# Optimization experiments

Measured on AMD Instinct MI355X. Metric: run time of the kernel, lower is better.

## Reference

```python
import jax, jax.numpy as jnp
import numpy as np

B, N, D, H, DH = 4, 4096, 1024, 8, 64
INNER = H * DH
EPS = 1e-5


def setup_inputs() -> dict:
    key = jax.random.key(0)
    ks = jax.random.split(key, 8)
    x = jax.random.normal(ks[0], (B, N, D), dtype=jnp.float32)
    W_qkv = jax.random.normal(ks[1], (3 * INNER, D), dtype=jnp.float32) * 0.02
    gamma_q = 1.0 + 0.1 * jax.random.normal(ks[2], (H, DH), dtype=jnp.float32)
    beta_q = 0.1 * jax.random.normal(ks[3], (H, DH), dtype=jnp.float32)
    gamma_k = 1.0 + 0.1 * jax.random.normal(ks[4], (H, DH), dtype=jnp.float32)
    beta_k = 0.1 * jax.random.normal(ks[5], (H, DH), dtype=jnp.float32)
    W_out = jax.random.normal(ks[6], (D, INNER), dtype=jnp.float32) * 0.02
    b_out = jnp.zeros((D,), dtype=jnp.float32)
    return {"x": x, "W_qkv": W_qkv, "gamma_q": gamma_q, "beta_q": beta_q,
            "gamma_k": gamma_k, "beta_k": beta_k, "W_out": W_out, "b_out": b_out}


def _per_head_layernorm(t, gamma, beta):
    # t: [B, H, N, DH]; gamma/beta: [H, DH] (one LayerNorm per head)
    m = jnp.mean(t, axis=-1, keepdims=True)
    var = jnp.mean(jnp.square(t - m), axis=-1, keepdims=True)
    tn = (t - m) * jax.lax.rsqrt(var + EPS)
    return tn * gamma[None, :, None, :] + beta[None, :, None, :]


def reference(x, W_qkv, gamma_q, beta_q, gamma_k, beta_k, W_out, b_out):
    b, n, d = x.shape
    h, dh = gamma_q.shape
    qkv = x @ W_qkv.T                                   # [B, N, 3*H*DH]
    q, k, v = jnp.split(qkv, 3, axis=-1)
    to_heads = lambda t: t.reshape(b, n, h, dh).transpose(0, 2, 1, 3)  # [B,H,N,DH]
    q, k, v = to_heads(q), to_heads(k), to_heads(v)
    q = _per_head_layernorm(q, gamma_q, beta_q)
    k = _per_head_layernorm(k, gamma_k, beta_k)
    # Softmax-free Galerkin attention: (Q K^T V) / (sqrt(dh) * n) reassociated
    # as Q (K^T V) -- mathematically identical, linear in n.
    scale = 1.0 / (jnp.sqrt(jnp.asarray(dh, x.dtype)) * n)
    kv = jnp.einsum('bhnd,bhne->bhde', k, v)            # [B,H,DH,DH]
    out = jnp.einsum('bhnd,bhde->bhne', q, kv) * scale  # [B,H,N,DH]
    out = out.transpose(0, 2, 1, 3).reshape(b, n, h * dh)
    return out @ W_out.T + b_out
```

## Files before the change

### kernel.cpp

```cpp
#include <hip/hip_runtime.h>
#include <stdint.h>

typedef unsigned short u16;
typedef unsigned int u32;
typedef __bf16 bf16x8 __attribute__((ext_vector_type(8)));
typedef float f32x4 __attribute__((ext_vector_type(4)));

__device__ __forceinline__ float bf2f(u16 u) {
  return __builtin_bit_cast(float, (u32)u << 16);
}
__device__ __forceinline__ u16 f2b(float f) {
  u32 u = __builtin_bit_cast(u32, f);
  u32 r = (u + 0x7fffu + ((u >> 16) & 1u)) >> 16;
  return (u16)r;
}
__device__ __forceinline__ void gload16(const u16* g, u16* l) {
  __builtin_amdgcn_global_load_lds(
      (const __attribute__((address_space(1))) u32*)(const void*)g,
      (__attribute__((address_space(3))) u32*)(void*)l, 16, 0, 0);
}
__device__ __forceinline__ void unpack16(uint4 a, uint4 b, float* o) {
  u32 w[8] = {a.x, a.y, a.z, a.w, b.x, b.y, b.z, b.w};
#pragma unroll
  for (int i = 0; i < 8; ++i) {
    o[2 * i]     = __builtin_bit_cast(float, w[i] << 16);
    o[2 * i + 1] = __builtin_bit_cast(float, w[i] & 0xffff0000u);
  }
}

__global__ __launch_bounds__(256) void cvt_bf16(const float* __restrict__ in,
                                                u16* __restrict__ out, int n4) {
  int i = blockIdx.x * 256 + threadIdx.x;
  if (i >= n4) return;
  float4 v = reinterpret_cast<const float4*>(in)[i];
  ushort4 o;
  o.x = f2b(v.x); o.y = f2b(v.y); o.z = f2b(v.z); o.w = f2b(v.w);
  reinterpret_cast<ushort4*>(out)[i] = o;
}

template <int MODE>
__global__ __launch_bounds__(256, 3) void gemm_bt(
    const u16* __restrict__ A, const u16* __restrict__ B, void* __restrict__ C,
    const float* __restrict__ gq, const float* __restrict__ bq,
    const float* __restrict__ gk, const float* __restrict__ bk,
    const float* __restrict__ bias, int M, int N, int K, int ntn) {
  __shared__ u16 As[2][128 * 32];
  __shared__ u16 Bs[2][128 * 32];

  const int nwg = gridDim.x;
  const int bid0 = blockIdx.x;
  const int bid = (bid0 & 7) * (nwg >> 3) + (bid0 >> 3);
  const int tm = bid / ntn, tn = bid % ntn;
  const int brow = tm << 7, bcol = tn << 7;
  const int tid = threadIdx.x;
  const int w = tid >> 6, lane = tid & 63;
  const int wrow = (w >> 1) << 6, wcol = (w & 1) << 6;
  const int lr = lane & 15, lg = lane >> 4;

  const int sslot = (lane & 3) ^ ((lane >> 3) & 3);
  const u16* Asrc = A + (size_t)(brow + (lane >> 2)) * K + sslot * 8;
  const u16* Bsrc = B + (size_t)(bcol + (lane >> 2)) * K + sslot * 8;

  auto stage = [&](int t, int buf) {
    const int k0 = t << 5;
#pragma unroll
    for (int i = 0; i < 2; ++i) {
      int g = w + 4 * i;
      gload16(Asrc + (size_t)(16 * g) * K + k0, &As[buf][(16 * g) * 32]);
      gload16(Bsrc + (size_t)(16 * g) * K + k0, &Bs[buf][(16 * g) * 32]);
    }
  };

  f32x4 acc[4][4];
#pragma unroll
  for (int m = 0; m < 4; ++m)
#pragma unroll
    for (int n = 0; n < 4; ++n) acc[m][n] = (f32x4){0.f, 0.f, 0.f, 0.f};

  const int NC = K >> 5;
  const int kslot = (lg ^ ((lr >> 1) & 3)) << 3;

  stage(0, 0);
  __syncthreads();

  for (int t = 0; t < NC; ++t) {
    const int cur = t & 1;
    if (t + 1 < NC) stage(t + 1, cur ^ 1);

    const u16* Asb = As[cur];
    const u16* Bsb = Bs[cur];
    bf16x8 af[4], bfr[4];
#pragma unroll
    for (int m = 0; m < 4; ++m)
      af[m] = *reinterpret_cast<const bf16x8*>(&Asb[(wrow + m * 16 + lr) * 32 + kslot]);
#pragma unroll
    for (int n = 0; n < 4; ++n)
      bfr[n] = *reinterpret_cast<const bf16x8*>(&Bsb[(wcol + n * 16 + lr) * 32 + kslot]);
    __builtin_amdgcn_s_setprio(1);
#pragma unroll
    for (int m = 0; m < 4; ++m)
#pragma unroll
      for (int n = 0; n < 4; ++n)
        acc[m][n] = __builtin_amdgcn_mfma_f32_16x16x32_bf16(af[m], bfr[n], acc[m][n], 0, 0, 0);
    __builtin_amdgcn_s_setprio(0);
    __syncthreads();
  }

  const int orow = brow + wrow + ((lane >> 4) << 2);
  const int ocol = bcol + wcol + lr;
  if (MODE == 0) {
    const int wcol0 = bcol + wcol;
    const int sect = wcol0 >> 6;
    const bool doln = sect < 16;
    const float* Gp = (sect < 8) ? (gq + wcol0) : (gk + (wcol0 - 512));
    const float* Pp = (sect < 8) ? (bq + wcol0) : (bk + (wcol0 - 512));
    float gv[4], pv[4];
    if (doln) {
#pragma unroll
      for (int n = 0; n < 4; ++n) { gv[n] = Gp[n * 16 + lr]; pv[n] = Pp[n * 16 + lr]; }
    }
    u16* Cp = (u16*)C;
#pragma unroll
    for (int m = 0; m < 4; ++m)
#pragma unroll
      for (int r = 0; r < 4; ++r) {
        size_t rowoff = (size_t)(orow + m * 16 + r) * N;
        if (doln) {
          float s = 0.f, s2 = 0.f;
#pragma unroll
          for (int n = 0; n < 4; ++n) {
            float x = acc[m][n][r];
            s += x; s2 += x * x;
          }
#pragma unroll
          for (int off = 8; off; off >>= 1) {
            s += __shfl_xor(s, off, 64);
            s2 += __shfl_xor(s2, off, 64);
          }
          float mean = s * 0.015625f;
          float inv = rsqrtf(s2 * 0.015625f - mean * mean + 1e-5f);
#pragma unroll
          for (int n = 0; n < 4; ++n)
            Cp[rowoff + ocol + n * 16] =
                f2b((acc[m][n][r] - mean) * inv * gv[n] + pv[n]);
        } else {
#pragma unroll
          for (int n = 0; n < 4; ++n)
            Cp[rowoff + ocol + n * 16] = f2b(acc[m][n][r]);
        }
      }
  } else {
    float bvv[4];
#pragma unroll
    for (int n = 0; n < 4; ++n) bvv[n] = bias[ocol + n * 16];
    float* Cp = (float*)C;
#pragma unroll
    for (int m = 0; m < 4; ++m)
#pragma unroll
      for (int r = 0; r < 4; ++r) {
        size_t rowoff = (size_t)(orow + m * 16 + r) * N;
#pragma unroll
        for (int n = 0; n < 4; ++n)
          Cp[rowoff + ocol + n * 16] = acc[m][n][r] + bvv[n];
      }
  }
}

__global__ __launch_bounds__(256) void kv_accum(const u16* __restrict__ qkv,
                                                float* __restrict__ KV) {
  int nch = blockIdx.x & 7;
  int bh = blockIdx.x >> 3;
  int b = bh >> 3, h = bh & 7;
  __shared__ float ks[64][64];
  __shared__ float vs[64][64];
  int tid = threadIdx.x;
  int ty = tid >> 4, tx = tid & 15;
  int rr = tid >> 2, cc = (tid & 3) * 16;
  float acc[4][4];
#pragma unroll
  for (int i = 0; i < 4; ++i)
#pragma unroll
    for (int j = 0; j < 4; ++j) acc[i][j] = 0.f;

  for (int t = 0; t < 8; ++t) {
    int n0 = nch * 512 + t * 64;
    __syncthreads();
    size_t base = ((size_t)(b * 4096 + n0 + rr)) * 1536 + h * 64 + cc;
    const uint4* kp = reinterpret_cast<const uint4*>(&qkv[base + 512]);
    const uint4* vp = reinterpret_cast<const uint4*>(&qkv[base + 1024]);
    uint4 k0 = kp[0], k1 = kp[1];
    uint4 v0 = vp[0], v1 = vp[1];
    unpack16(k0, k1, &ks[rr][cc]);
    unpack16(v0, v1, &vs[rr][cc]);
    __syncthreads();
    for (int n = 0; n < 64; ++n) {
      float4 k4 = *reinterpret_cast<const float4*>(&ks[n][ty * 4]);
      float4 v4 = *reinterpret_cast<const float4*>(&vs[n][tx * 4]);
      float ka[4] = {k4.x, k4.y, k4.z, k4.w};
      float va[4] = {v4.x, v4.y, v4.z, v4.w};
#pragma unroll
      for (int i = 0; i < 4; ++i)
#pragma unroll
        for (int j = 0; j < 4; ++j) acc[i][j] += ka[i] * va[j];
    }
  }
  float* dst = KV + (size_t)bh * 4096;
#pragma unroll
  for (int i = 0; i < 4; ++i)
#pragma unroll
    for (int j = 0; j < 4; ++j)
      atomicAdd(&dst[(ty * 4 + i) * 64 + tx * 4 + j], acc[i][j]);
}

__global__ __launch_bounds__(256) void attn_kernel(const u16* __restrict__ qkv,
                                                   const float* __restrict__ KV,
                                                   u16* __restrict__ attn) {
  int rblk = blockIdx.x;
  int b = rblk >> 6;
  __shared__ float qs[64][65];
  __shared__ float kvs[64][64];
  int tid = threadIdx.x;
  int ty = tid >> 4, tx = tid & 15;
  int rr = tid >> 2, cc = (tid & 3) * 16;
  const float scale = 1.0f / 32768.0f;
  for (int h = 0; h < 8; ++h) {
    __syncthreads();
    size_t qbase = ((size_t)(rblk * 64 + rr)) * 1536 + h * 64 + cc;
    const uint4* qp = reinterpret_cast<const uint4*>(&qkv[qbase]);
    uint4 q0 = qp[0], q1 = qp[1];
    unpack16(q0, q1, &qs[rr][cc]);
    const float4* kp =
        reinterpret_cast<const float4*>(&KV[((size_t)(b * 8 + h)) * 4096 + rr * 64 + cc]);
#pragma unroll
    for (int j = 0; j < 4; ++j) {
      float4 t = kp[j];
      kvs[rr][cc + 4 * j + 0] = t.x;
      kvs[rr][cc + 4 * j + 1] = t.y;
      kvs[rr][cc + 4 * j + 2] = t.z;
      kvs[rr][cc + 4 * j + 3] = t.w;
    }
    __syncthreads();
    float acc[4][4] = {};
    for (int d = 0; d < 64; ++d) {
      float a0 = qs[ty * 4 + 0][d], a1 = qs[ty * 4 + 1][d];
      float a2 = qs[ty * 4 + 2][d], a3 = qs[ty * 4 + 3][d];
      float4 bv = *reinterpret_cast<const float4*>(&kvs[d][tx * 4]);
      float ba[4] = {bv.x, bv.y, bv.z, bv.w};
#pragma unroll
      for (int j = 0; j < 4; ++j) {
        acc[0][j] += a0 * ba[j];
        acc[1][j] += a1 * ba[j];
        acc[2][j] += a2 * ba[j];
        acc[3][j] += a3 * ba[j];
      }
    }
#pragma unroll
    for (int i = 0; i < 4; ++i) {
      int row = rblk * 64 + ty * 4 + i;
      ushort4 o;
      o.x = f2b(acc[i][0] * scale);
      o.y = f2b(acc[i][1] * scale);
      o.z = f2b(acc[i][2] * scale);
      o.w = f2b(acc[i][3] * scale);
      *reinterpret_cast<ushort4*>(&attn[(size_t)row * 512 + h * 64 + tx * 4]) = o;
    }
  }
}

extern "C" void kernel_launch(void* const* d_in, const int* in_sizes, int n_in,
                              void* d_out, int out_size, void* d_ws, size_t ws_size,
                              hipStream_t stream) {
  const float* x  = (const float*)d_in[0];
  const float* Wq = (const float*)d_in[1];
  const float* gq = (const float*)d_in[2];
  const float* bq = (const float*)d_in[3];
  const float* gk = (const float*)d_in[4];
  const float* bk = (const float*)d_in[5];
  const float* Wo = (const float*)d_in[6];
  const float* bo = (const float*)d_in[7];
  float* out = (float*)d_out;

  char* p = (char*)d_ws;
  auto carve = [&](size_t bytes) {
    char* r = p;
    p += (bytes + 255) & ~(size_t)255;
    return r;
  };
  u16* xb    = (u16*)carve((size_t)16384 * 1024 * 2);
  u16* wqb   = (u16*)carve((size_t)1536 * 1024 * 2);
  u16* wob   = (u16*)carve((size_t)1024 * 512 * 2);
  u16* qkv   = (u16*)carve((size_t)16384 * 1536 * 2);
  float* KVb = (float*)carve((size_t)32 * 64 * 64 * 4);
  u16* attn  = (u16*)carve((size_t)16384 * 512 * 2);

  hipMemsetAsync(KVb, 0, (size_t)32 * 64 * 64 * 4, stream);
  cvt_bf16<<<16384, 256, 0, stream>>>(x, xb, 4194304);
  cvt_bf16<<<1536, 256, 0, stream>>>(Wq, wqb, 393216);
  cvt_bf16<<<512, 256, 0, stream>>>(Wo, wob, 131072);
  gemm_bt<0><<<128 * 12, 256, 0, stream>>>(xb, wqb, qkv, gq, bq, gk, bk, nullptr,
                                           16384, 1536, 1024, 12);
  kv_accum<<<256, 256, 0, stream>>>(qkv, KVb);
  attn_kernel<<<256, 256, 0, stream>>>(qkv, KVb, attn);
  gemm_bt<1><<<128 * 8, 256, 0, stream>>>(attn, wob, out, nullptr, nullptr, nullptr,
                                          nullptr, bo, 16384, 1024, 512, 8);
}
```

Baseline: 189.2 us.

## Fold KV into output projection weights, drop attention intermediate pass

Instead of computing Q·KV into a bf16 attention buffer and then multiplying by W_out, a small per-batch kernel precomputes W2[b] = (KV[b]·W_out-slice)^T scaled, and the output GEMM reads Q directly from the qkv buffer (strided lda) with a per-batch B matrix. This removes the attn_kernel and its 16 MB intermediate write and read. kv_accum is split into twice as many blocks for more parallelism, and the GEMM occupancy hint is raised from 3 to 4. The folded weights are rounded to bf16, which changes rounding slightly.

```diff
diff --git a/kernel.cpp b/kernel.cpp
--- a/kernel.cpp
+++ b/kernel.cpp
@@ -39,11 +39,12 @@
 }
 
 template <int MODE>
-__global__ __launch_bounds__(256, 3) void gemm_bt(
+__global__ __launch_bounds__(256, 4) void gemm_bt(
     const u16* __restrict__ A, const u16* __restrict__ B, void* __restrict__ C,
     const float* __restrict__ gq, const float* __restrict__ bq,
     const float* __restrict__ gk, const float* __restrict__ bk,
-    const float* __restrict__ bias, int M, int N, int K, int ntn) {
+    const float* __restrict__ bias, int M, int N, int K, int ntn,
+    int lda, size_t bstride) {
   __shared__ u16 As[2][128 * 32];
   __shared__ u16 Bs[2][128 * 32];
 
@@ -57,16 +58,18 @@
   const int wrow = (w >> 1) << 6, wcol = (w & 1) << 6;
   const int lr = lane & 15, lg = lane >> 4;
 
+  const u16* Bp = (MODE == 1) ? (B + (size_t)(brow >> 12) * bstride) : B;
+
   const int sslot = (lane & 3) ^ ((lane >> 3) & 3);
-  const u16* Asrc = A + (size_t)(brow + (lane >> 2)) * K + sslot * 8;
-  const u16* Bsrc = B + (size_t)(bcol + (lane >> 2)) * K + sslot * 8;
+  const u16* Asrc = A + (size_t)(brow + (lane >> 2)) * lda + sslot * 8;
+  const u16* Bsrc = Bp + (size_t)(bcol + (lane >> 2)) * K + sslot * 8;
 
   auto stage = [&](int t, int buf) {
     const int k0 = t << 5;
 #pragma unroll
     for (int i = 0; i < 2; ++i) {
       int g = w + 4 * i;
-      gload16(Asrc + (size_t)(16 * g) * K + k0, &As[buf][(16 * g) * 32]);
+      gload16(Asrc + (size_t)(16 * g) * lda + k0, &As[buf][(16 * g) * 32]);
       gload16(Bsrc + (size_t)(16 * g) * K + k0, &Bs[buf][(16 * g) * 32]);
     }
   };
@@ -168,8 +171,8 @@
 
 __global__ __launch_bounds__(256) void kv_accum(const u16* __restrict__ qkv,
                                                 float* __restrict__ KV) {
-  int nch = blockIdx.x & 7;
-  int bh = blockIdx.x >> 3;
+  int nch = blockIdx.x & 15;
+  int bh = blockIdx.x >> 4;
   int b = bh >> 3, h = bh & 7;
   __shared__ float ks[64][64];
   __shared__ float vs[64][64];
@@ -182,8 +185,8 @@
 #pragma unroll
     for (int j = 0; j < 4; ++j) acc[i][j] = 0.f;
 
-  for (int t = 0; t < 8; ++t) {
-    int n0 = nch * 512 + t * 64;
+  for (int t = 0; t < 4; ++t) {
+    int n0 = nch * 256 + t * 64;
     __syncthreads();
     size_t base = ((size_t)(b * 4096 + n0 + rr)) * 1536 + h * 64 + cc;
     const uint4* kp = reinterpret_cast<const uint4*>(&qkv[base + 512]);
@@ -212,58 +215,48 @@
       atomicAdd(&dst[(ty * 4 + i) * 64 + tx * 4 + j], acc[i][j]);
 }
 
-__global__ __launch_bounds__(256) void attn_kernel(const u16* __restrict__ qkv,
-                                                   const float* __restrict__ KV,
-                                                   u16* __restrict__ attn) {
-  int rblk = blockIdx.x;
-  int b = rblk >> 6;
-  __shared__ float qs[64][65];
+__global__ __launch_bounds__(256) void w2_kernel(const float* __restrict__ KV,
+                                                 const u16* __restrict__ wob,
+                                                 u16* __restrict__ w2) {
+  int bh = blockIdx.x & 31, jt = blockIdx.x >> 5;
+  int b = bh >> 3, h = bh & 7;
   __shared__ float kvs[64][64];
-  int tid = threadIdx.x;
-  int ty = tid >> 4, tx = tid & 15;
-  int rr = tid >> 2, cc = (tid & 3) * 16;
+  int t = threadIdx.x;
+  {
+    const float4* src = reinterpret_cast<const float4*>(KV + (size_t)bh * 4096);
+    float4* dst = reinterpret_cast<float4*>(&kvs[0][0]);
+#pragma unroll
+    for (int i = 0; i < 4; ++i) dst[t + 256 * i] = src[t + 256 * i];
+  }
+  __syncthreads();
+  int jloc = t & 127, dg = t >> 7;
+  int j = jt * 128 + jloc;
+  float wo[64];
+  const u16* wr = wob + (size_t)j * 512 + h * 64;
+#pragma unroll
+  for (int e8 = 0; e8 < 8; ++e8) {
+    uint4 pk = *reinterpret_cast<const uint4*>(wr + e8 * 8);
+    u32 wds[4] = {pk.x, pk.y, pk.z, pk.w};
+#pragma unroll
+    for (int i = 0; i < 4; ++i) {
+      wo[e8 * 8 + 2 * i]     = bf2f((u16)(wds[i] & 0xffffu));
+      wo[e8 * 8 + 2 * i + 1] = bf2f((u16)(wds[i] >> 16));
+    }
+  }
   const float scale = 1.0f / 32768.0f;
-  for (int h = 0; h < 8; ++h) {
-    __syncthreads();
-    size_t qbase = ((size_t)(rblk * 64 + rr)) * 1536 + h * 64 + cc;
-    const uint4* qp = reinterpret_cast<const uint4*>(&qkv[qbase]);
-    uint4 q0 = qp[0], q1 = qp[1];
-    unpack16(q0, q1, &qs[rr][cc]);
-    const float4* kp =
-        reinterpret_cast<const float4*>(&KV[((size_t)(b * 8 + h)) * 4096 + rr * 64 + cc]);
-#pragma unroll
-    for (int j = 0; j < 4; ++j) {
-      float4 t = kp[j];
-      kvs[rr][cc + 4 * j + 0] = t.x;
-      kvs[rr][cc + 4 * j + 1] = t.y;
-      kvs[rr][cc + 4 * j + 2] = t.z;
-      kvs[rr][cc + 4 * j + 3] = t.w;
-    }
-    __syncthreads();
-    float acc[4][4] = {};
-    for (int d = 0; d < 64; ++d) {
-      float a0 = qs[ty * 4 + 0][d], a1 = qs[ty * 4 + 1][d];
-      float a2 = qs[ty * 4 + 2][d], a3 = qs[ty * 4 + 3][d];
-      float4 bv = *reinterpret_cast<const float4*>(&kvs[d][tx * 4]);
-      float ba[4] = {bv.x, bv.y, bv.z, bv.w};
-#pragma unroll
-      for (int j = 0; j < 4; ++j) {
-        acc[0][j] += a0 * ba[j];
-        acc[1][j] += a1 * ba[j];
-        acc[2][j] += a2 * ba[j];
-        acc[3][j] += a3 * ba[j];
-      }
-    }
-#pragma unroll
-    for (int i = 0; i < 4; ++i) {
-      int row = rblk * 64 + ty * 4 + i;
-      ushort4 o;
-      o.x = f2b(acc[i][0] * scale);
-      o.y = f2b(acc[i][1] * scale);
-      o.z = f2b(acc[i][2] * scale);
-      o.w = f2b(acc[i][3] * scale);
-      *reinterpret_cast<ushort4*>(&attn[(size_t)row * 512 + h * 64 + tx * 4]) = o;
-    }
+  u16* outp = w2 + ((size_t)b * 1024 + j) * 512 + h * 64 + dg * 32;
+#pragma unroll
+  for (int dd = 0; dd < 32; ++dd) {
+    int d = dg * 32 + dd;
+    float acc = 0.f;
+    const float4* kr = reinterpret_cast<const float4*>(&kvs[d][0]);
+#pragma unroll
+    for (int e4 = 0; e4 < 16; ++e4) {
+      float4 kv4 = kr[e4];
+      acc += kv4.x * wo[e4 * 4] + kv4.y * wo[e4 * 4 + 1] +
+             kv4.z * wo[e4 * 4 + 2] + kv4.w * wo[e4 * 4 + 3];
+    }
+    outp[dd] = f2b(acc * scale);
   }
 }
 
@@ -291,16 +284,17 @@
   u16* wob   = (u16*)carve((size_t)1024 * 512 * 2);
   u16* qkv   = (u16*)carve((size_t)16384 * 1536 * 2);
   float* KVb = (float*)carve((size_t)32 * 64 * 64 * 4);
-  u16* attn  = (u16*)carve((size_t)16384 * 512 * 2);
+  u16* w2b   = (u16*)carve((size_t)4 * 1024 * 512 * 2);
 
   hipMemsetAsync(KVb, 0, (size_t)32 * 64 * 64 * 4, stream);
   cvt_bf16<<<16384, 256, 0, stream>>>(x, xb, 4194304);
   cvt_bf16<<<1536, 256, 0, stream>>>(Wq, wqb, 393216);
   cvt_bf16<<<512, 256, 0, stream>>>(Wo, wob, 131072);
   gemm_bt<0><<<128 * 12, 256, 0, stream>>>(xb, wqb, qkv, gq, bq, gk, bk, nullptr,
-                                           16384, 1536, 1024, 12);
-  kv_accum<<<256, 256, 0, stream>>>(qkv, KVb);
-  attn_kernel<<<256, 256, 0, stream>>>(qkv, KVb, attn);
-  gemm_bt<1><<<128 * 8, 256, 0, stream>>>(attn, wob, out, nullptr, nullptr, nullptr,
-                                          nullptr, bo, 16384, 1024, 512, 8);
-}
+                                           16384, 1536, 1024, 12, 1024, 0);
+  kv_accum<<<512, 256, 0, stream>>>(qkv, KVb);
+  w2_kernel<<<256, 256, 0, stream>>>(KVb, wob, w2b);
+  gemm_bt<1><<<128 * 8, 256, 0, stream>>>(qkv, w2b, out, nullptr, nullptr, nullptr,
+                                          nullptr, bo, 16384, 1024, 512, 8,
+                                          1536, (size_t)1024 * 512);
+}
```

After: 179.8 us. 1.05x faster.
